# Optimization experiments

Measured on AMD Instinct MI355X. Metric: run time of the kernel, lower is better.

## Reference

```python
import jax, jax.numpy as jnp
import numpy as np

B = 2048   # num_trajectories
T = 32     # rollout
I = 1024   # input_size
H = 1024   # hidden_size


def setup_inputs() -> dict:
    key = jax.random.key(0)
    ks = jax.random.split(key, 5)
    head_output = jax.random.normal(ks[0], (B * T, I), jnp.float32)
    rnn_states = jax.random.normal(ks[1], (B, 2 * H), jnp.float32)
    dones = (jax.random.uniform(ks[2], (B * T,)) < 0.05).astype(jnp.float32)
    s = 1.0 / np.sqrt(H)
    w_ih = jax.random.uniform(ks[3], (4 * H, I), jnp.float32, -s, s)
    w_hh = jax.random.uniform(ks[4], (4 * H, H), jnp.float32, -s, s)
    b_ih = jnp.zeros((4 * H,), jnp.float32)  # initialize() fills biases with 0
    b_hh = jnp.zeros((4 * H,), jnp.float32)
    return {"head_output": head_output, "rnn_states": rnn_states, "dones": dones,
            "w_ih": w_ih, "w_hh": w_hh, "b_ih": b_ih, "b_hh": b_hh, "rollout": T}


def reference(head_output, rnn_states, dones, w_ih, w_hh, b_ih, b_hh, rollout):
    # is_seq=True path, n_rnn_layer=1
    n_traj = head_output.shape[0] // rollout
    Hh = rnn_states.shape[1] // 2
    h0, c0 = rnn_states[:, :Hh], rnn_states[:, Hh:]          # [B,H] each
    x = head_output.reshape(n_traj, rollout, -1).transpose(1, 0, 2)  # [T,B,I]
    # is_new_episode = roll(dones, 1, time); first step never resets
    resets = jnp.roll(dones.reshape(n_traj, rollout), 1, axis=1).at[:, 0].set(0.0).T  # [T,B]
    # Precompute the input GEMM for all timesteps in one big matmul
    x_gates = jnp.einsum('tbi,gi->tbg', x, w_ih) + b_ih + b_hh  # [T,B,4H]

    def step(carry, inp):
        h, c = carry
        xg, r = inp
        keep = (1.0 - r)[:, None]
        h = h * keep
        c = c * keep
        gates = xg + h @ w_hh.T                                # [B,4H]
        i, f, g, o = jnp.split(gates, 4, axis=1)               # torch gate order i,f,g,o
        i = jax.nn.sigmoid(i)
        f = jax.nn.sigmoid(f)
        g = jnp.tanh(g)
        o = jax.nn.sigmoid(o)
        c = f * c + i * g
        h = o * jnp.tanh(c)
        return (h, c), h

    (h, c), outs = jax.lax.scan(step, (h0, c0), (x_gates, resets))
    x_out = outs.transpose(1, 0, 2).reshape(n_traj * rollout, -1)  # permute(1,0,2).flatten(0,1)
    new_rnn_states = jnp.concatenate([h, c], axis=1)               # [B,2H]
    return x_out, new_rnn_states
```

## Files before the change

kernel.cpp:

```cpp
#include <hip/hip_runtime.h>
#include <stdint.h>

typedef __attribute__((ext_vector_type(8))) short short8;
typedef __attribute__((ext_vector_type(4))) float f32x4;

#define NTRAJ 2048
#define TSTEP 32
#define HDIM  1024
#define KCAT  2048
#define NGATE 4096

__device__ __forceinline__ unsigned short f2bf(float f) {
  union { float f; unsigned int u; } v; v.f = f;
  unsigned int u = v.u + 0x7FFFu + ((v.u >> 16) & 1u);
  return (unsigned short)(u >> 16);
}
__device__ __forceinline__ float sigmoidf_(float x) {
  return 1.0f / (1.0f + __expf(-x));
}
__device__ __forceinline__ float tanhf_(float x) {
  return 1.0f - 2.0f / (__expf(2.0f * x) + 1.0f);
}


__global__ void cvt_bf16_kernel(const float* __restrict__ src,
                                unsigned short* __restrict__ dst, int n4) {
  int i = blockIdx.x * blockDim.x + threadIdx.x;
  if (i >= n4) return;
  float4 v = ((const float4*)src)[i];
  ushort4 o;
  o.x = f2bf(v.x); o.y = f2bf(v.y); o.z = f2bf(v.z); o.w = f2bf(v.w);
  ((ushort4*)dst)[i] = o;
}

__global__ void wcat_kernel(const float* __restrict__ wih,
                            const float* __restrict__ whh,
                            unsigned short* __restrict__ wcat) {
  int i = blockIdx.x * blockDim.x + threadIdx.x;
  int e = i * 4;
  int row = e >> 11;
  int col = e & 2047;
  const float* src = (col < 1024) ? (wih + (size_t)row * 1024 + col)
                                  : (whh + (size_t)row * 1024 + (col - 1024));
  float4 v = *(const float4*)src;
  ushort4 o;
  o.x = f2bf(v.x); o.y = f2bf(v.y); o.z = f2bf(v.z); o.w = f2bf(v.w);
  ((ushort4*)wcat)[i] = o;
}

__global__ void state_prep(const float* __restrict__ rnn,
                           const float* __restrict__ bih,
                           const float* __restrict__ bhh,
                           unsigned short* __restrict__ h0,
                           float* __restrict__ c0,
                           float* __restrict__ bias) {
  int i = blockIdx.x * blockDim.x + threadIdx.x;
  int b = i >> 10, j = i & 1023;
  float hv = rnn[(size_t)b * 2048 + j];
  float cv = rnn[(size_t)b * 2048 + 1024 + j];
  h0[i] = f2bf(hv);
  c0[i] = cv;
  if (i < 4096) bias[i] = bih[i] + bhh[i];
}

__global__ __launch_bounds__(256, 2)
void lstm_step(const unsigned short* __restrict__ X,
               const unsigned short* __restrict__ Wcat,
               const float* __restrict__ bias,
               const float* __restrict__ dones,
               const unsigned short* __restrict__ h_in,
               unsigned short* __restrict__ h_out,
               float* __restrict__ cbuf,
               float* __restrict__ out,
               float* __restrict__ rnn_out,
               int t) {
  __shared__ union __align__(16) ShMem {
    struct { unsigned short A[64 * 32]; unsigned short Bt[4 * 64 * 32]; } st;
    float gates[4][64 * 64];
  } sh;

  const int tid  = threadIdx.x;
  const int wave = tid >> 6;
  const int lane = tid & 63;
  const int l16  = lane & 15;
  const int quad = lane >> 4;
  const int bBase = blockIdx.x * 64;
  const int n0    = blockIdx.y * 64;

  f32x4 acc[4][4];
#pragma unroll
  for (int nt = 0; nt < 4; ++nt) {
    float bv = bias[wave * 1024 + n0 + nt * 16 + l16];
    f32x4 in4 = {bv, bv, bv, bv};
#pragma unroll
    for (int mt = 0; mt < 4; ++mt) acc[mt][nt] = in4;
  }

  const int ra = tid >> 2;
  const int ca = (tid & 3) * 8;

  for (int kk = 0; kk < 64; ++kk) {
    const int k0 = kk * 32;
    const unsigned short* asrc;
    if (k0 < 1024)
      asrc = X + ((size_t)(bBase + ra) * 32 + t) * 1024 + k0 + ca;
    else
      asrc = h_in + (size_t)(bBase + ra) * 1024 + (k0 - 1024) + ca;
    *(uint4*)&sh.st.A[ra * 32 + ca] = *(const uint4*)asrc;
#pragma unroll
    for (int q = 0; q < 4; ++q) {
      int e = (q * 256 + tid) * 8;
      int g = e >> 11;
      int rem = e & 2047;
      int rb = rem >> 5, cb = rem & 31;
      const unsigned short* bsrc =
          Wcat + (size_t)(g * 1024 + n0 + rb) * 2048 + k0 + cb;
      *(uint4*)&sh.st.Bt[e] = *(const uint4*)bsrc;
    }
    __syncthreads();

    short8 fa[4], fb[4];
#pragma unroll
    for (int mt = 0; mt < 4; ++mt)
      fa[mt] = *(const short8*)&sh.st.A[(mt * 16 + l16) * 32 + quad * 8];
#pragma unroll
    for (int nt = 0; nt < 4; ++nt)
      fb[nt] = *(const short8*)&sh.st.Bt[(wave * 64 + nt * 16 + l16) * 32 + quad * 8];
#pragma unroll
    for (int mt = 0; mt < 4; ++mt)
#pragma unroll
      for (int nt = 0; nt < 4; ++nt)
        acc[mt][nt] = __builtin_amdgcn_mfma_f32_16x16x32_bf16(fa[mt], fb[nt],
                                                              acc[mt][nt], 0, 0, 0);
    __syncthreads();
  }

#pragma unroll
  for (int mt = 0; mt < 4; ++mt)
#pragma unroll
    for (int nt = 0; nt < 4; ++nt)
#pragma unroll
      for (int v = 0; v < 4; ++v)
        sh.gates[wave][(mt * 16 + quad * 4 + v) * 64 + nt * 16 + l16] =
            acc[mt][nt][v];
  __syncthreads();

  const int mrow = tid >> 6;
  const int n = tid & 63;
#pragma unroll 4
  for (int it = 0; it < 16; ++it) {
    int m = it * 4 + mrow;
    int b = bBase + m;
    int j = n0 + n;
    float gi = sigmoidf_(sh.gates[0][m * 64 + n]);
    float gf = sigmoidf_(sh.gates[1][m * 64 + n]);
    float gg = tanhf_  (sh.gates[2][m * 64 + n]);
    float go = sigmoidf_(sh.gates[3][m * 64 + n]);
    float cold = cbuf[(size_t)b * 1024 + j];
    float cn = gf * cold + gi * gg;
    float hn = go * tanhf_(cn);
    out[((size_t)b * 32 + t) * 1024 + j] = hn;
    float keep = (t < 31) ? (1.0f - dones[b * 32 + t]) : 1.0f;
    cbuf[(size_t)b * 1024 + j] = cn * keep;
    h_out[(size_t)b * 1024 + j] = f2bf(hn * keep);
    if (t == 31) {
      rnn_out[(size_t)b * 2048 + j] = hn;
      rnn_out[(size_t)b * 2048 + 1024 + j] = cn;
    }
  }
}

extern "C" void kernel_launch(void* const* d_in, const int* in_sizes, int n_in,
                              void* d_out, int out_size, void* d_ws, size_t ws_size,
                              hipStream_t stream) {
  (void)in_sizes; (void)n_in; (void)out_size; (void)ws_size;
  const float* head  = (const float*)d_in[0];
  const float* rnn   = (const float*)d_in[1];
  const float* dones = (const float*)d_in[2];
  const float* wih   = (const float*)d_in[3];
  const float* whh   = (const float*)d_in[4];
  const float* bih   = (const float*)d_in[5];
  const float* bhh   = (const float*)d_in[6];
  float* out = (float*)d_out;
  float* rnn_out = out + (size_t)65536 * 1024;

  char* ws = (char*)d_ws;
  unsigned short* X    = (unsigned short*)(ws);
  unsigned short* Wcat = (unsigned short*)(ws + 134217728);
  float*          bias = (float*)(ws + 150994944);
  unsigned short* h0   = (unsigned short*)(ws + 151011328);
  unsigned short* h1   = (unsigned short*)(ws + 155205632);
  float*          cbuf = (float*)(ws + 159399936);

  cvt_bf16_kernel<<<65536, 256, 0, stream>>>(head, X, 16777216);
  wcat_kernel<<<8192, 256, 0, stream>>>(wih, whh, Wcat);
  state_prep<<<8192, 256, 0, stream>>>(rnn, bih, bhh, h0, cbuf, bias);

  unsigned short* hb[2] = {h0, h1};
  for (int t = 0; t < TSTEP; ++t) {
    lstm_step<<<dim3(32, 16), 256, 0, stream>>>(
        X, Wcat, bias, dones, hb[t & 1], hb[(t + 1) & 1], cbuf, out, rnn_out, t);
  }
}
```

Baseline: 2.897 ms.

## Use async global-to-LDS loads, time-major X layout, and in-register gate epilogue

The bf16 conversion kernel now writes X in time-major order so each step's A-tile rows are contiguous. Tile loads switch from register-staged copies to global_load_lds direct-to-LDS transfers. The N tiling is remapped so each wave holds all four gates for its 16 columns, which lets the LSTM cell update run straight from accumulators without the shared-memory gate staging pass. Loads are still not double-buffered, so each k-step keeps its two barriers.

```diff
diff --git a/kernel.cpp b/kernel.cpp
--- a/kernel.cpp
+++ b/kernel.cpp
@@ -22,15 +22,26 @@
   return 1.0f - 2.0f / (__expf(2.0f * x) + 1.0f);
 }
 
+__device__ __forceinline__ void async_lds16(const void* g, void* l) {
+  __builtin_amdgcn_global_load_lds(
+      (const __attribute__((address_space(1))) unsigned int*)g,
+      (__attribute__((address_space(3))) unsigned int*)l, 16, 0, 0);
+}
+
 
 __global__ void cvt_bf16_kernel(const float* __restrict__ src,
                                 unsigned short* __restrict__ dst, int n4) {
   int i = blockIdx.x * blockDim.x + threadIdx.x;
   if (i >= n4) return;
   float4 v = ((const float4*)src)[i];
+  int e = i * 4;
+  int row = e >> 10;
+  int col = e & 1023;
+  int traj = row >> 5, tt = row & 31;
+  size_t de = (((size_t)tt * 2048 + traj) << 10) + col;
   ushort4 o;
   o.x = f2bf(v.x); o.y = f2bf(v.y); o.z = f2bf(v.z); o.w = f2bf(v.w);
-  ((ushort4*)dst)[i] = o;
+  *(ushort4*)&dst[de] = o;
 }
 
 __global__ void wcat_kernel(const float* __restrict__ wih,
@@ -74,10 +85,8 @@
                float* __restrict__ out,
                float* __restrict__ rnn_out,
                int t) {
-  __shared__ union __align__(16) ShMem {
-    struct { unsigned short A[64 * 32]; unsigned short Bt[4 * 64 * 32]; } st;
-    float gates[4][64 * 64];
-  } sh;
+  __shared__ __align__(16) unsigned short Atile[64 * 32];
+  __shared__ __align__(16) unsigned short Btile[4 * 64 * 32];
 
   const int tid  = threadIdx.x;
   const int wave = tid >> 6;
@@ -87,85 +96,85 @@
   const int bBase = blockIdx.x * 64;
   const int n0    = blockIdx.y * 64;
 
+  const int col = n0 + wave * 16 + l16;
+
   f32x4 acc[4][4];
 #pragma unroll
-  for (int nt = 0; nt < 4; ++nt) {
-    float bv = bias[wave * 1024 + n0 + nt * 16 + l16];
-    f32x4 in4 = {bv, bv, bv, bv};
-#pragma unroll
-    for (int mt = 0; mt < 4; ++mt) acc[mt][nt] = in4;
-  }
-
-  const int ra = tid >> 2;
-  const int ca = (tid & 3) * 8;
-
-  for (int kk = 0; kk < 64; ++kk) {
-    const int k0 = kk * 32;
-    const unsigned short* asrc;
-    if (k0 < 1024)
-      asrc = X + ((size_t)(bBase + ra) * 32 + t) * 1024 + k0 + ca;
-    else
-      asrc = h_in + (size_t)(bBase + ra) * 1024 + (k0 - 1024) + ca;
-    *(uint4*)&sh.st.A[ra * 32 + ca] = *(const uint4*)asrc;
-#pragma unroll
-    for (int q = 0; q < 4; ++q) {
-      int e = (q * 256 + tid) * 8;
-      int g = e >> 11;
-      int rem = e & 2047;
-      int rb = rem >> 5, cb = rem & 31;
-      const unsigned short* bsrc =
-          Wcat + (size_t)(g * 1024 + n0 + rb) * 2048 + k0 + cb;
-      *(uint4*)&sh.st.Bt[e] = *(const uint4*)bsrc;
-    }
+  for (int g = 0; g < 4; ++g) {
+    float bv = bias[g * 1024 + col];
+    f32x4 b4 = {bv, bv, bv, bv};
+#pragma unroll
+    for (int mt = 0; mt < 4; ++mt) acc[mt][g] = b4;
+  }
+
+  const int lr = lane >> 2;
+  const int lc = (lane & 3) * 8;
+  const unsigned short* aX =
+      X + (((size_t)t * 2048) + bBase + wave * 16 + lr) * 1024 + lc;
+  const unsigned short* aH =
+      h_in + (size_t)(bBase + wave * 16 + lr) * 1024 + lc;
+  unsigned short* aD = &Atile[wave * 512];
+
+  const unsigned short* bS[4];
+  unsigned short* bD[4];
+#pragma unroll
+  for (int q = 0; q < 4; ++q) {
+    int cb = wave + 4 * q;
+    int g  = cb >> 2;
+    int row = g * 1024 + n0 + (cb & 3) * 16 + lr;
+    bS[q] = Wcat + (size_t)row * 2048 + lc;
+    bD[q] = &Btile[cb * 512];
+  }
+
+  auto kstep = [&](const unsigned short*& asrc) {
+    async_lds16(asrc, aD);
+#pragma unroll
+    for (int q = 0; q < 4; ++q) async_lds16(bS[q], bD[q]);
     __syncthreads();
 
     short8 fa[4], fb[4];
 #pragma unroll
     for (int mt = 0; mt < 4; ++mt)
-      fa[mt] = *(const short8*)&sh.st.A[(mt * 16 + l16) * 32 + quad * 8];
-#pragma unroll
-    for (int nt = 0; nt < 4; ++nt)
-      fb[nt] = *(const short8*)&sh.st.Bt[(wave * 64 + nt * 16 + l16) * 32 + quad * 8];
+      fa[mt] = *(const short8*)&Atile[(mt * 16 + l16) * 32 + quad * 8];
+#pragma unroll
+    for (int g = 0; g < 4; ++g)
+      fb[g] = *(const short8*)&Btile[(g * 64 + wave * 16 + l16) * 32 + quad * 8];
 #pragma unroll
     for (int mt = 0; mt < 4; ++mt)
 #pragma unroll
-      for (int nt = 0; nt < 4; ++nt)
-        acc[mt][nt] = __builtin_amdgcn_mfma_f32_16x16x32_bf16(fa[mt], fb[nt],
-                                                              acc[mt][nt], 0, 0, 0);
+      for (int g = 0; g < 4; ++g)
+        acc[mt][g] = __builtin_amdgcn_mfma_f32_16x16x32_bf16(fa[mt], fb[g],
+                                                             acc[mt][g], 0, 0, 0);
     __syncthreads();
-  }
-
-#pragma unroll
-  for (int mt = 0; mt < 4; ++mt)
-#pragma unroll
-    for (int nt = 0; nt < 4; ++nt)
-#pragma unroll
-      for (int v = 0; v < 4; ++v)
-        sh.gates[wave][(mt * 16 + quad * 4 + v) * 64 + nt * 16 + l16] =
-            acc[mt][nt][v];
-  __syncthreads();
-
-  const int mrow = tid >> 6;
-  const int n = tid & 63;
-#pragma unroll 4
-  for (int it = 0; it < 16; ++it) {
-    int m = it * 4 + mrow;
-    int b = bBase + m;
-    int j = n0 + n;
-    float gi = sigmoidf_(sh.gates[0][m * 64 + n]);
-    float gf = sigmoidf_(sh.gates[1][m * 64 + n]);
-    float gg = tanhf_  (sh.gates[2][m * 64 + n]);
-    float go = sigmoidf_(sh.gates[3][m * 64 + n]);
-    float cold = cbuf[(size_t)b * 1024 + j];
-    float cn = gf * cold + gi * gg;
-    float hn = go * tanhf_(cn);
-    out[((size_t)b * 32 + t) * 1024 + j] = hn;
-    float keep = (t < 31) ? (1.0f - dones[b * 32 + t]) : 1.0f;
-    cbuf[(size_t)b * 1024 + j] = cn * keep;
-    h_out[(size_t)b * 1024 + j] = f2bf(hn * keep);
-    if (t == 31) {
-      rnn_out[(size_t)b * 2048 + j] = hn;
-      rnn_out[(size_t)b * 2048 + 1024 + j] = cn;
+
+    asrc += 32;
+#pragma unroll
+    for (int q = 0; q < 4; ++q) bS[q] += 32;
+  };
+
+  for (int kk = 0; kk < 32; ++kk) kstep(aX);
+  for (int kk = 0; kk < 32; ++kk) kstep(aH);
+
+#pragma unroll
+  for (int mt = 0; mt < 4; ++mt) {
+#pragma unroll
+    for (int v = 0; v < 4; ++v) {
+      int b = bBase + mt * 16 + quad * 4 + v;
+      float gi = sigmoidf_(acc[mt][0][v]);
+      float gf = sigmoidf_(acc[mt][1][v]);
+      float gg = tanhf_  (acc[mt][2][v]);
+      float go = sigmoidf_(acc[mt][3][v]);
+      float cold = cbuf[(size_t)b * 1024 + col];
+      float cn = gf * cold + gi * gg;
+      float hn = go * tanhf_(cn);
+      out[((size_t)b * 32 + t) * 1024 + col] = hn;
+      float keep = (t < 31) ? (1.0f - dones[b * 32 + t]) : 1.0f;
+      cbuf[(size_t)b * 1024 + col] = cn * keep;
+      h_out[(size_t)b * 1024 + col] = f2bf(hn * keep);
+      if (t == 31) {
+        rnn_out[(size_t)b * 2048 + col] = hn;
+        rnn_out[(size_t)b * 2048 + 1024 + col] = cn;
+      }
     }
   }
 }
```

After: 2.863 ms. About the same (-1.2%).
